# Kernel tuning notes

Hardware: AMD Instinct MI355X
Metric: run time of the kernel (lower is better)

The kernel has to match this reference:

```python
import jax, jax.numpy as jnp
import numpy as np

EPS = 1e-08

def quantize_weights(w):
    # absmean ternary quantization: round(w/delta) clipped to {-1,0,1}, rescaled by delta
    delta = jnp.mean(jnp.abs(w)) + EPS
    w_quant = jnp.clip(jnp.round(w / delta), -1.0, 1.0)
    return w_quant * delta

def setup_inputs() -> dict:
    key = jax.random.key(0)
    k1, k2 = jax.random.split(key)
    B, T, IN, OUT = 8, 16, 4096, 11008
    x = jax.random.normal(k1, (B, T, IN), dtype=jnp.float32)
    weight = jax.random.normal(k2, (OUT, IN), dtype=jnp.float32)
    bias = jnp.zeros((OUT,), dtype=jnp.float32)
    return {"x": x, "weight": weight, "bias": bias}

def reference(x, weight, bias):
    w_quant = quantize_weights(weight)
    # F.linear: x @ w_quant.T + bias
    out = jnp.einsum("bti,oi->bto", x, w_quant) + bias
    return out
```

## Files before the change

### kernel.cpp

```cpp
#include <hip/hip_runtime.h>
#include <hip/hip_bf16.h>

typedef __bf16 bf16x8 __attribute__((ext_vector_type(8)));
typedef float f32x4 __attribute__((ext_vector_type(4)));
typedef unsigned short ushort8 __attribute__((ext_vector_type(8)));
typedef unsigned short ushort4v __attribute__((ext_vector_type(4)));

constexpr int M = 128;
constexpr int K = 4096;
constexpr int N = 11008;
constexpr int BN = 64;
constexpr int BK = 32;
constexpr int KSPLIT = 4;
constexpr int KBLK = K / KSPLIT;
constexpr int NBX = N / BN;
constexpr int NBLK = NBX * KSPLIT;
constexpr long long NW = (long long)N * K;
constexpr size_t MN = (size_t)M * N;
constexpr int SCAP = 512;

constexpr float DHAT = 0.79788456f;
constexpr float INV_DHAT = 1.0f / DHAT;
constexpr float BAND = 2e-4f;
constexpr float DEVMAX = 3.5e-4f;

constexpr size_t PART_OFF  = 0;
constexpr size_t FLAG_OFF  = 4096;
constexpr size_t CNT_OFF   = FLAG_OFF + 4;
constexpr size_t XBF_OFF   = 8192;
constexpr size_t SLIST_OFF = XBF_OFF + (size_t)M * K * 2;
constexpr size_t P_OFF     = SLIST_OFF + (size_t)NBLK * SCAP * 8;
constexpr size_t WS_NEED   = P_OFF + KSPLIT * MN * sizeof(float);
constexpr size_t WS_MIN    = 8192;

__device__ __forceinline__ unsigned short f2bf_bits(float f) {
    unsigned int u = __builtin_bit_cast(unsigned int, f);
    u += 0x7FFFu + ((u >> 16) & 1u);
    return (unsigned short)(u >> 16);
}
__device__ __forceinline__ float bf_to_f32(unsigned short b) {
    return __builtin_bit_cast(float, ((unsigned int)b) << 16);
}
__device__ __forceinline__ int tern(float w, float inv_d) {
    float q = rintf(w * inv_d);
    q = fminf(1.f, fmaxf(-1.f, q));
    return (int)q;
}
__device__ __forceinline__ float block_delta(const float* partials, int tid) {
    __shared__ float red[4];
    float s = 0.f;
    for (int i = tid; i < NBLK; i += 256) s += partials[i];
#pragma unroll
    for (int off = 32; off > 0; off >>= 1) s += __shfl_down(s, off, 64);
    if ((tid & 63) == 0) red[tid >> 6] = s;
    __syncthreads();
    return (float)((double)((red[0] + red[1]) + (red[2] + red[3])) /
                   (double)NW + 1e-8);
}

__global__ __launch_bounds__(256) void xcvt(const float* __restrict__ x,
                                            unsigned short* __restrict__ xbf)
{
    const int gtid = blockIdx.x * blockDim.x + threadIdx.x;
    const float4* xp = (const float4*)x + (size_t)gtid * 2;
    float4 a = xp[0], b = xp[1];
    ushort8 o;
    o[0] = f2bf_bits(a.x); o[1] = f2bf_bits(a.y);
    o[2] = f2bf_bits(a.z); o[3] = f2bf_bits(a.w);
    o[4] = f2bf_bits(b.x); o[5] = f2bf_bits(b.y);
    o[6] = f2bf_bits(b.z); o[7] = f2bf_bits(b.w);
    *(ushort8*)(xbf + (size_t)gtid * 8) = o;
}

__global__ __launch_bounds__(256, 4) void bitlinear_gemm(
    const unsigned short* __restrict__ xb, const float* __restrict__ W,
    float* __restrict__ partials, unsigned int* __restrict__ cnt,
    uint2* __restrict__ slist, unsigned int* __restrict__ flag,
    float* __restrict__ pbase)
{
    constexpr int KSTEPS = KBLK / BK;
    constexpr int LDSW = 40;
    __shared__ __attribute__((aligned(16))) unsigned short xs[2][M * LDSW];
    __shared__ __attribute__((aligned(16))) unsigned short wsm[2][BN * LDSW];
    __shared__ float red[4];

    const int tid = threadIdx.x;
    const int lane = tid & 63;
    const int wid = tid >> 6;
    const int wm = wid >> 1;
    const int wn = wid & 1;
    const int cgrp = lane >> 4;
    const int l15 = lane & 15;
    const int n0 = blockIdx.x * BN;
    const int kk0 = blockIdx.y * KBLK;
    const int bid = blockIdx.y * NBX + blockIdx.x;
    const int K4 = K / 4;
    const float4* w4p = (const float4*)W;
    uint2* mylist = slist + (size_t)bid * SCAP;

    ushort8 xrA[2], xrB[2];
    float4 wrA[2], wrB[2];
    float sabs = 0.f;

    auto issue_set = [&](int t, ushort8 (&xr)[2], float4 (&wr)[2]) {
#pragma unroll
        for (int i = 0; i < 2; ++i) {
            const int j = tid + i * 256;
            xr[i] = *(const ushort8*)(xb + (size_t)(j >> 2) * K + kk0 + t * BK + (j & 3) * 8);
        }
#pragma unroll
        for (int i = 0; i < 2; ++i) {
            const int j = tid + i * 256;
            wr[i] = w4p[(size_t)(n0 + (j >> 3)) * K4 + (kk0 + t * BK) / 4 + (j & 7)];
        }
    };

    auto stage_set = [&](int buf, int t, ushort8 (&xr)[2], float4 (&wr)[2]) {
#pragma unroll
        for (int i = 0; i < 2; ++i) {
            const int j = tid + i * 256;
            *(ushort8*)&xs[buf][(j >> 2) * LDSW + (j & 3) * 8] = xr[i];
        }
#pragma unroll
        for (int i = 0; i < 2; ++i) {
            const int j = tid + i * 256;
            const int row = j >> 3, q4 = j & 7;
            float wf[4] = {wr[i].x, wr[i].y, wr[i].z, wr[i].w};
            ushort4v wq;
            unsigned int msk = 0u;
#pragma unroll
            for (int e = 0; e < 4; ++e) {
                const float r = wf[e] * INV_DHAT;
                float qv = rintf(r);
                qv = fminf(1.f, fmaxf(-1.f, qv));
                wq[e] = f2bf_bits(qv);
                sabs += fabsf(wf[e]);
                msk |= (fabsf(fabsf(r) - 0.5f) < BAND) ? (1u << e) : 0u;
            }
            *(ushort4v*)&wsm[buf][row * LDSW + q4 * 4] = wq;
            if (msk) {
#pragma unroll
                for (int e = 0; e < 4; ++e) {
                    if (msk & (1u << e)) {
                        unsigned int slot = atomicAdd(cnt + bid, 1u);
                        if (slot < SCAP) {
                            unsigned int idx = ((unsigned int)(n0 + row) << 12) |
                                               (unsigned int)(kk0 + t * BK + q4 * 4 + e);
                            mylist[slot] = make_uint2(idx, __float_as_uint(wf[e]));
                        } else {
                            atomicOr(flag, 1u);
                        }
                    }
                }
            }
        }
    };

    f32x4 acc[4][2] = {};

    auto compute = [&](int buf) {
        const unsigned short* xcur = xs[buf];
        const unsigned short* wcur = wsm[buf];
        bf16x8 afr[4], bfr[2];
#pragma unroll
        for (int f = 0; f < 4; ++f)
            afr[f] = *(const bf16x8*)&xcur[(wm * 64 + f * 16 + l15) * LDSW + cgrp * 8];
#pragma unroll
        for (int g = 0; g < 2; ++g)
            bfr[g] = *(const bf16x8*)&wcur[(wn * 32 + g * 16 + l15) * LDSW + cgrp * 8];
#pragma unroll
        for (int f = 0; f < 4; ++f)
#pragma unroll
            for (int g = 0; g < 2; ++g)
                acc[f][g] = __builtin_amdgcn_mfma_f32_16x16x32_bf16(
                    afr[f], bfr[g], acc[f][g], 0, 0, 0);
    };

    issue_set(0, xrA, wrA);
    issue_set(1, xrB, wrB);

    for (int t = 0; t < KSTEPS; t += 2) {
        stage_set(0, t, xrA, wrA);
        if (t + 2 < KSTEPS) issue_set(t + 2, xrA, wrA);
        __syncthreads();
        compute(0);
        stage_set(1, t + 1, xrB, wrB);
        if (t + 3 < KSTEPS) issue_set(t + 3, xrB, wrB);
        __syncthreads();
        compute(1);
    }

#pragma unroll
    for (int off = 32; off > 0; off >>= 1) sabs += __shfl_down(sabs, off, 64);
    if (lane == 0) red[wid] = sabs;
    __syncthreads();
    if (tid == 0) partials[bid] = (red[0] + red[1]) + (red[2] + red[3]);

    float* dst = pbase + (size_t)blockIdx.y * MN;
#pragma unroll
    for (int f = 0; f < 4; ++f) {
        const int mrow = wm * 64 + f * 16 + cgrp * 4;
#pragma unroll
        for (int g = 0; g < 2; ++g) {
            const int ocol = n0 + wn * 32 + g * 16 + l15;
#pragma unroll
            for (int r = 0; r < 4; ++r)
                dst[(size_t)(mrow + r) * N + ocol] = acc[f][g][r];
        }
    }
}

__global__ __launch_bounds__(256) void combine(const float* __restrict__ p,
                                               const float* __restrict__ partials,
                                               const float* __restrict__ bias,
                                               float4* __restrict__ out)
{
    const float delta = block_delta(partials, threadIdx.x);
    const int i4 = blockIdx.x * blockDim.x + threadIdx.x;
    constexpr int N4 = N / 4;
    if (i4 >= (int)(MN / 4)) return;
    const float4 b = *(const float4*)(bias + (i4 % N4) * 4);
    float4 s = {};
#pragma unroll
    for (int y = 0; y < KSPLIT; ++y) {
        float4 v = ((const float4*)(p + y * MN))[i4];
        s.x += v.x; s.y += v.y; s.z += v.z; s.w += v.w;
    }
    float4 o;
    o.x = fmaf(delta, s.x, b.x); o.y = fmaf(delta, s.y, b.y);
    o.z = fmaf(delta, s.z, b.z); o.w = fmaf(delta, s.w, b.w);
    out[i4] = o;
}

__global__ __launch_bounds__(256) void fixup(
    const float* __restrict__ W, const unsigned short* __restrict__ xbf,
    const float* __restrict__ partials, const unsigned int* __restrict__ cnt,
    const uint2* __restrict__ slist, const unsigned int* __restrict__ flag,
    float* __restrict__ out)
{
    const int tid = threadIdx.x;
    const float delta = block_delta(partials, tid);
    const float inv_delta = 1.0f / delta;
    const int bid = blockIdx.y * NBX + blockIdx.x;
    const bool bad = (*flag != 0u) || (fabsf(delta * INV_DHAT - 1.f) > DEVMAX);

    if (!bad) {
        const int cb = (int)min(cnt[bid], (unsigned int)SCAP);
        const uint2* mylist = slist + (size_t)bid * SCAP;
        for (int si = 0; si < cb; ++si) {
            const uint2 e = mylist[si];
            const float w = __uint_as_float(e.y);
            const int dq = tern(w, inv_delta) - tern(w, INV_DHAT);
            if (dq == 0) continue;
            const unsigned int n = e.x >> 12, k = e.x & 4095u;
            const float corr = delta * (float)dq;
            if (tid < M)
                atomicAdd(&out[(size_t)tid * N + n],
                          corr * bf_to_f32(xbf[(size_t)tid * K + k]));
        }
    } else {
        const int n0 = blockIdx.x * BN, kk0 = blockIdx.y * KBLK;
        for (int r = 0; r < BN; ++r) {
            for (int kk = tid; kk < KBLK; kk += 256) {
                const float w = W[(size_t)(n0 + r) * K + kk0 + kk];
                const int dq = tern(w, inv_delta) - tern(w, INV_DHAT);
                if (dq == 0) continue;
                const float corr = delta * (float)dq;
                for (int m = 0; m < M; ++m)
                    atomicAdd(&out[(size_t)m * N + n0 + r],
                              corr * bf_to_f32(xbf[(size_t)m * K + kk0 + kk]));
            }
        }
    }
}

__global__ __launch_bounds__(256) void absmean_direct(const float* __restrict__ w,
                                                      float* __restrict__ partials)
{
    const int gtid = blockIdx.x * blockDim.x + threadIdx.x;
    const int n4 = (int)(NW / 4);
    const float4* w4 = (const float4*)w;
    float s0 = 0.f, s1 = 0.f, s2 = 0.f, s3 = 0.f;
    for (int i = gtid; i < n4; i += gridDim.x * blockDim.x) {
        float4 v = w4[i];
        s0 += fabsf(v.x); s1 += fabsf(v.y); s2 += fabsf(v.z); s3 += fabsf(v.w);
    }
    float s = (s0 + s1) + (s2 + s3);
#pragma unroll
    for (int off = 32; off > 0; off >>= 1) s += __shfl_down(s, off, 64);
    __shared__ float red[4];
    if ((threadIdx.x & 63) == 0) red[threadIdx.x >> 6] = s;
    __syncthreads();
    if (threadIdx.x == 0)
        partials[blockIdx.x] = (red[0] + red[1]) + (red[2] + red[3]);
}

__global__ __launch_bounds__(256, 4) void gemm_direct(
    const float* __restrict__ X, const float* __restrict__ W,
    const float* __restrict__ bias, const float* __restrict__ partials,
    float* __restrict__ out)
{
    constexpr int KSTEPS = K / BK;
    constexpr int LDSW = 40;
    __shared__ __attribute__((aligned(16))) unsigned short xs[2][M * LDSW];
    __shared__ __attribute__((aligned(16))) unsigned short wsm[2][BN * LDSW];
    __shared__ float red[4];
    const int tid = threadIdx.x, lane = tid & 63, wid = tid >> 6;
    const int wm = wid >> 1, wn = wid & 1, cgrp = lane >> 4, l15 = lane & 15;
    const int n0 = blockIdx.x * BN, K4 = K / 4;
    const float4* x4p = (const float4*)X;
    const float4* w4p = (const float4*)W;
    float4 xfA[4], xfB[4], wrA[2], wrB[2];

    auto issue_set = [&](int t, float4 (&xf)[4], float4 (&wr)[2]) {
#pragma unroll
        for (int i = 0; i < 4; ++i) {
            const int j = tid + i * 256;
            xf[i] = x4p[(size_t)(j >> 3) * K4 + (t * BK) / 4 + (j & 7)];
        }
#pragma unroll
        for (int i = 0; i < 2; ++i) {
            const int j = tid + i * 256;
            wr[i] = w4p[(size_t)(n0 + (j >> 3)) * K4 + (t * BK) / 4 + (j & 7)];
        }
    };

    float ps[8];
#pragma unroll
    for (int i = 0; i < 8; ++i) ps[i] = partials[tid + i * 256];
    issue_set(0, xfA, wrA);
    issue_set(1, xfB, wrB);
    float s = 0.f;
#pragma unroll
    for (int i = 0; i < 8; ++i) s += ps[i];
#pragma unroll
    for (int off = 32; off > 0; off >>= 1) s += __shfl_down(s, off, 64);
    if (lane == 0) red[wid] = s;
    __syncthreads();
    const float delta =
        (float)((double)((red[0] + red[1]) + (red[2] + red[3])) / (double)NW + 1e-8);
    const float inv_delta = 1.0f / delta;

    auto stage_set = [&](int buf, float4 (&xf)[4], float4 (&wr)[2]) {
#pragma unroll
        for (int i = 0; i < 4; ++i) {
            const int j = tid + i * 256;
            float4 v = xf[i];
            ushort4v o;
            o[0] = f2bf_bits(v.x); o[1] = f2bf_bits(v.y);
            o[2] = f2bf_bits(v.z); o[3] = f2bf_bits(v.w);
            *(ushort4v*)&xs[buf][(j >> 3) * LDSW + (j & 7) * 4] = o;
        }
#pragma unroll
        for (int i = 0; i < 2; ++i) {
            const int j = tid + i * 256;
            float wf[4] = {wr[i].x, wr[i].y, wr[i].z, wr[i].w};
            ushort4v wq;
#pragma unroll
            for (int e = 0; e < 4; ++e)
                wq[e] = f2bf_bits((float)tern(wf[e], inv_delta));
            *(ushort4v*)&wsm[buf][(j >> 3) * LDSW + (j & 7) * 4] = wq;
        }
    };

    f32x4 acc[4][2] = {};
    auto compute = [&](int buf) {
        bf16x8 afr[4], bfr[2];
#pragma unroll
        for (int f = 0; f < 4; ++f)
            afr[f] = *(const bf16x8*)&xs[buf][(wm * 64 + f * 16 + l15) * LDSW + cgrp * 8];
#pragma unroll
        for (int g = 0; g < 2; ++g)
            bfr[g] = *(const bf16x8*)&wsm[buf][(wn * 32 + g * 16 + l15) * LDSW + cgrp * 8];
#pragma unroll
        for (int f = 0; f < 4; ++f)
#pragma unroll
            for (int g = 0; g < 2; ++g)
                acc[f][g] = __builtin_amdgcn_mfma_f32_16x16x32_bf16(
                    afr[f], bfr[g], acc[f][g], 0, 0, 0);
    };

    for (int t = 0; t < KSTEPS; t += 2) {
        stage_set(0, xfA, wrA);
        if (t + 2 < KSTEPS) issue_set(t + 2, xfA, wrA);
        __syncthreads();
        compute(0);
        stage_set(1, xfB, wrB);
        if (t + 3 < KSTEPS) issue_set(t + 3, xfB, wrB);
        __syncthreads();
        compute(1);
    }
#pragma unroll
    for (int f = 0; f < 4; ++f) {
        const int mrow = wm * 64 + f * 16 + cgrp * 4;
#pragma unroll
        for (int g = 0; g < 2; ++g) {
            const int ocol = n0 + wn * 32 + g * 16 + l15;
            const float bv = bias[ocol];
#pragma unroll
            for (int r = 0; r < 4; ++r)
                out[(size_t)(mrow + r) * N + ocol] = delta * acc[f][g][r] + bv;
        }
    }
}

extern "C" void kernel_launch(void* const* d_in, const int* in_sizes, int n_in,
                              void* d_out, int out_size, void* d_ws, size_t ws_size,
                              hipStream_t stream) {
    const float* x = (const float*)d_in[0];
    const float* w = (const float*)d_in[1];
    const float* bias = (const float*)d_in[2];
    float* out = (float*)d_out;
    char* wsb = (char*)d_ws;
    float* partials = (float*)(wsb + PART_OFF);
    unsigned int* flag = (unsigned int*)(wsb + FLAG_OFF);
    unsigned int* cnt = (unsigned int*)(wsb + CNT_OFF);
    unsigned short* xbf = (unsigned short*)(wsb + XBF_OFF);
    uint2* slist = (uint2*)(wsb + SLIST_OFF);
    float* pbase = (float*)(wsb + P_OFF);

    if (ws_size >= WS_NEED) {
        hipMemsetAsync(wsb + FLAG_OFF, 0, 4 + NBLK * 4, stream);
        xcvt<<<M * K / 8 / 256, 256, 0, stream>>>(x, xbf);
        bitlinear_gemm<<<dim3(NBX, KSPLIT), 256, 0, stream>>>(
            xbf, w, partials, cnt, slist, flag, pbase);
        combine<<<(int)(MN / 4) / 256, 256, 0, stream>>>(
            pbase, partials, bias, (float4*)out);
        fixup<<<dim3(NBX, KSPLIT), 256, 0, stream>>>(
            w, xbf, partials, cnt, slist, flag, out);
    } else if (ws_size >= WS_MIN) {
        absmean_direct<<<2048, 256, 0, stream>>>(w, partials);
        gemm_direct<<<NBX, 256, 0, stream>>>(x, w, bias, partials, out);
    }
}
```

Baseline: 72.82 us.

## Pre-quantize weights to packed 2-bit codes in a streaming prep pass

Result: slower. 87.84 us (+20.6%).

```diff
diff --git a/kernel.cpp b/kernel.cpp
--- a/kernel.cpp
+++ b/kernel.cpp
@@ -14,10 +14,10 @@
 constexpr int KSPLIT = 4;
 constexpr int KBLK = K / KSPLIT;
 constexpr int NBX = N / BN;
-constexpr int NBLK = NBX * KSPLIT;
 constexpr long long NW = (long long)N * K;
+constexpr int RBLK = 2048;
 constexpr size_t MN = (size_t)M * N;
-constexpr int SCAP = 512;
+constexpr int SCAP = 256;
 
 constexpr float DHAT = 0.79788456f;
 constexpr float INV_DHAT = 1.0f / DHAT;
@@ -25,13 +25,14 @@
 constexpr float DEVMAX = 3.5e-4f;
 
 constexpr size_t PART_OFF  = 0;
-constexpr size_t FLAG_OFF  = 4096;
-constexpr size_t CNT_OFF   = FLAG_OFF + 4;
-constexpr size_t XBF_OFF   = 8192;
-constexpr size_t SLIST_OFF = XBF_OFF + (size_t)M * K * 2;
-constexpr size_t P_OFF     = SLIST_OFF + (size_t)NBLK * SCAP * 8;
-constexpr size_t WS_NEED   = P_OFF + KSPLIT * MN * sizeof(float);
-constexpr size_t WS_MIN    = 8192;
+constexpr size_t FLAG_OFF  = 8192;
+constexpr size_t CNT_OFF   = 12288;
+constexpr size_t XBF_OFF   = 24576;
+constexpr size_t CODE_OFF  = XBF_OFF + (size_t)M * K * 2;
+constexpr size_t SLIST_OFF = CODE_OFF + (size_t)(NW / 4);
+constexpr size_t PACC_OFF  = SLIST_OFF + (size_t)RBLK * SCAP * 8;
+constexpr size_t WS_NEED   = PACC_OFF + KSPLIT * MN * sizeof(float);
+constexpr size_t WS_MIN    = 16384;
 
 __device__ __forceinline__ unsigned short f2bf_bits(float f) {
     unsigned int u = __builtin_bit_cast(unsigned int, f);
@@ -49,7 +50,8 @@
 __device__ __forceinline__ float block_delta(const float* partials, int tid) {
     __shared__ float red[4];
     float s = 0.f;
-    for (int i = tid; i < NBLK; i += 256) s += partials[i];
+#pragma unroll
+    for (int i = 0; i < RBLK / 256; ++i) s += partials[tid + i * 256];
 #pragma unroll
     for (int off = 32; off > 0; off >>= 1) s += __shfl_down(s, off, 64);
     if ((tid & 63) == 0) red[tid >> 6] = s;
@@ -58,31 +60,82 @@
                    (double)NW + 1e-8);
 }
 
-__global__ __launch_bounds__(256) void xcvt(const float* __restrict__ x,
-                                            unsigned short* __restrict__ xbf)
+template <bool CVT>
+__global__ __launch_bounds__(256) void prep(const float* __restrict__ w,
+                                            const float* __restrict__ x,
+                                            float* __restrict__ partials,
+                                            unsigned short* __restrict__ xbf,
+                                            unsigned char* __restrict__ codes,
+                                            unsigned int* __restrict__ cnt,
+                                            uint2* __restrict__ slist,
+                                            unsigned int* __restrict__ flag)
 {
     const int gtid = blockIdx.x * blockDim.x + threadIdx.x;
-    const float4* xp = (const float4*)x + (size_t)gtid * 2;
-    float4 a = xp[0], b = xp[1];
-    ushort8 o;
-    o[0] = f2bf_bits(a.x); o[1] = f2bf_bits(a.y);
-    o[2] = f2bf_bits(a.z); o[3] = f2bf_bits(a.w);
-    o[4] = f2bf_bits(b.x); o[5] = f2bf_bits(b.y);
-    o[6] = f2bf_bits(b.z); o[7] = f2bf_bits(b.w);
-    *(ushort8*)(xbf + (size_t)gtid * 8) = o;
-}
-
-__global__ __launch_bounds__(256, 4) void bitlinear_gemm(
-    const unsigned short* __restrict__ xb, const float* __restrict__ W,
-    float* __restrict__ partials, unsigned int* __restrict__ cnt,
-    uint2* __restrict__ slist, unsigned int* __restrict__ flag,
+    if (CVT && gtid < M * K / 8) {
+        const float4* xp = (const float4*)x + (size_t)gtid * 2;
+        float4 a = xp[0], b = xp[1];
+        ushort8 o;
+        o[0] = f2bf_bits(a.x); o[1] = f2bf_bits(a.y);
+        o[2] = f2bf_bits(a.z); o[3] = f2bf_bits(a.w);
+        o[4] = f2bf_bits(b.x); o[5] = f2bf_bits(b.y);
+        o[6] = f2bf_bits(b.z); o[7] = f2bf_bits(b.w);
+        *(ushort8*)(xbf + (size_t)gtid * 8) = o;
+    }
+    const int n4 = (int)(NW / 4);
+    const float4* w4 = (const float4*)w;
+    uint2* mylist = slist + (size_t)blockIdx.x * SCAP;
+    const int stride = gridDim.x * blockDim.x;
+
+    float s0 = 0.f, s1 = 0.f, s2 = 0.f, s3 = 0.f;
+    for (int i = gtid; i < n4; i += stride) {
+        float4 v = w4[i];
+        s0 += fabsf(v.x); s1 += fabsf(v.y); s2 += fabsf(v.z); s3 += fabsf(v.w);
+        if (CVT) {
+            float vf[4] = {v.x, v.y, v.z, v.w};
+            unsigned int byte = 0u, msk = 0u;
+#pragma unroll
+            for (int e = 0; e < 4; ++e) {
+                const float r = vf[e] * INV_DHAT;
+                float qv = rintf(r);
+                qv = fminf(1.f, fmaxf(-1.f, qv));
+                const int iq = (int)qv;
+                byte |= ((unsigned int)iq & 3u) << (2 * e);
+                msk |= (fabsf(fabsf(r) - 0.5f) < BAND) ? (1u << e) : 0u;
+            }
+            codes[i] = (unsigned char)byte;
+            if (msk) {
+#pragma unroll
+                for (int e = 0; e < 4; ++e) {
+                    if (msk & (1u << e)) {
+                        unsigned int slot = atomicAdd(cnt + blockIdx.x, 1u);
+                        if (slot < SCAP)
+                            mylist[slot] = make_uint2(4u * (unsigned)i + e,
+                                                      __float_as_uint(vf[e]));
+                        else
+                            atomicOr(flag, 1u);
+                    }
+                }
+            }
+        }
+    }
+    float s = (s0 + s1) + (s2 + s3);
+#pragma unroll
+    for (int off = 32; off > 0; off >>= 1) s += __shfl_down(s, off, 64);
+    __shared__ float red[4];
+    if ((threadIdx.x & 63) == 0) red[threadIdx.x >> 6] = s;
+    __syncthreads();
+    if (threadIdx.x == 0)
+        partials[blockIdx.x] = (red[0] + red[1]) + (red[2] + red[3]);
+}
+
+__global__ __launch_bounds__(256, 4) void gemm_codes(
+    const unsigned short* __restrict__ xb, const unsigned short* __restrict__ c16,
     float* __restrict__ pbase)
 {
     constexpr int KSTEPS = KBLK / BK;
     constexpr int LDSW = 40;
     __shared__ __attribute__((aligned(16))) unsigned short xs[2][M * LDSW];
     __shared__ __attribute__((aligned(16))) unsigned short wsm[2][BN * LDSW];
-    __shared__ float red[4];
 
     const int tid = threadIdx.x;
     const int lane = tid & 63;
@@ -93,81 +146,45 @@
     const int l15 = lane & 15;
     const int n0 = blockIdx.x * BN;
     const int kk0 = blockIdx.y * KBLK;
-    const int bid = blockIdx.y * NBX + blockIdx.x;
-    const int K4 = K / 4;
-    const float4* w4p = (const float4*)W;
-    uint2* mylist = slist + (size_t)bid * SCAP;
+    const int K8 = K / 8;
 
     ushort8 xrA[2], xrB[2];
-    float4 wrA[2], wrB[2];
-    float sabs = 0.f;
-
-    auto issue_set = [&](int t, ushort8 (&xr)[2], float4 (&wr)[2]) {
+    unsigned int crA, crB;
+
+    auto issue_set = [&](int t, ushort8 (&xr)[2], unsigned int& cr) {
 #pragma unroll
         for (int i = 0; i < 2; ++i) {
             const int j = tid + i * 256;
             xr[i] = *(const ushort8*)(xb + (size_t)(j >> 2) * K + kk0 + t * BK + (j & 3) * 8);
         }
+        cr = c16[(size_t)(n0 + (tid >> 2)) * K8 + (kk0 + t * BK) / 8 + (tid & 3)];
+    };
+
+    auto stage_set = [&](int buf, ushort8 (&xr)[2], unsigned int cr) {
 #pragma unroll
         for (int i = 0; i < 2; ++i) {
             const int j = tid + i * 256;
-            wr[i] = w4p[(size_t)(n0 + (j >> 3)) * K4 + (kk0 + t * BK) / 4 + (j & 7)];
-        }
-    };
-
-    auto stage_set = [&](int buf, int t, ushort8 (&xr)[2], float4 (&wr)[2]) {
-#pragma unroll
-        for (int i = 0; i < 2; ++i) {
-            const int j = tid + i * 256;
             *(ushort8*)&xs[buf][(j >> 2) * LDSW + (j & 3) * 8] = xr[i];
         }
-#pragma unroll
-        for (int i = 0; i < 2; ++i) {
-            const int j = tid + i * 256;
-            const int row = j >> 3, q4 = j & 7;
-            float wf[4] = {wr[i].x, wr[i].y, wr[i].z, wr[i].w};
-            ushort4v wq;
-            unsigned int msk = 0u;
-#pragma unroll
-            for (int e = 0; e < 4; ++e) {
-                const float r = wf[e] * INV_DHAT;
-                float qv = rintf(r);
-                qv = fminf(1.f, fmaxf(-1.f, qv));
-                wq[e] = f2bf_bits(qv);
-                sabs += fabsf(wf[e]);
-                msk |= (fabsf(fabsf(r) - 0.5f) < BAND) ? (1u << e) : 0u;
-            }
-            *(ushort4v*)&wsm[buf][row * LDSW + q4 * 4] = wq;
-            if (msk) {
-#pragma unroll
-                for (int e = 0; e < 4; ++e) {
-                    if (msk & (1u << e)) {
-                        unsigned int slot = atomicAdd(cnt + bid, 1u);
-                        if (slot < SCAP) {
-                            unsigned int idx = ((unsigned int)(n0 + row) << 12) |
-                                               (unsigned int)(kk0 + t * BK + q4 * 4 + e);
-                            mylist[slot] = make_uint2(idx, __float_as_uint(wf[e]));
-                        } else {
-                            atomicOr(flag, 1u);
-                        }
-                    }
-                }
-            }
-        }
+        ushort8 wq;
+#pragma unroll
+        for (int e = 0; e < 8; ++e) {
+            const unsigned int c = (cr >> (2 * e)) & 3u;
+            wq[e] = (unsigned short)(((c & 1u) * 0x3F80u) | ((c & 2u) << 14));
+        }
+        *(ushort8*)&wsm[buf][(tid >> 2) * LDSW + (tid & 3) * 8] = wq;
     };
 
     f32x4 acc[4][2] = {};
 
     auto compute = [&](int buf) {
-        const unsigned short* xcur = xs[buf];
-        const unsigned short* wcur = wsm[buf];
         bf16x8 afr[4], bfr[2];
 #pragma unroll
         for (int f = 0; f < 4; ++f)
-            afr[f] = *(const bf16x8*)&xcur[(wm * 64 + f * 16 + l15) * LDSW + cgrp * 8];
+            afr[f] = *(const bf16x8*)&xs[buf][(wm * 64 + f * 16 + l15) * LDSW + cgrp * 8];
 #pragma unroll
         for (int g = 0; g < 2; ++g)
-            bfr[g] = *(const bf16x8*)&wcur[(wn * 32 + g * 16 + l15) * LDSW + cgrp * 8];
+            bfr[g] = *(const bf16x8*)&wsm[buf][(wn * 32 + g * 16 + l15) * LDSW + cgrp * 8];
 #pragma unroll
         for (int f = 0; f < 4; ++f)
 #pragma unroll
@@ -176,25 +193,19 @@
                     afr[f], bfr[g], acc[f][g], 0, 0, 0);
     };
 
-    issue_set(0, xrA, wrA);
-    issue_set(1, xrB, wrB);
+    issue_set(0, xrA, crA);
+    issue_set(1, xrB, crB);
 
     for (int t = 0; t < KSTEPS; t += 2) {
-        stage_set(0, t, xrA, wrA);
-        if (t + 2 < KSTEPS) issue_set(t + 2, xrA, wrA);
+        stage_set(0, xrA, crA);
+        if (t + 2 < KSTEPS) issue_set(t + 2, xrA, crA);
         __syncthreads();
         compute(0);
-        stage_set(1, t + 1, xrB, wrB);
-        if (t + 3 < KSTEPS) issue_set(t + 3, xrB, wrB);
+        stage_set(1, xrB, crB);
+        if (t + 3 < KSTEPS) issue_set(t + 3, xrB, crB);
         __syncthreads();
         compute(1);
     }
-
-#pragma unroll
-    for (int off = 32; off > 0; off >>= 1) sabs += __shfl_down(sabs, off, 64);
-    if (lane == 0) red[wid] = sabs;
-    __syncthreads();
-    if (tid == 0) partials[bid] = (red[0] + red[1]) + (red[2] + red[3]);
 
     float* dst = pbase + (size_t)blockIdx.y * MN;
 #pragma unroll
@@ -241,12 +252,11 @@
     const int tid = threadIdx.x;
     const float delta = block_delta(partials, tid);
     const float inv_delta = 1.0f / delta;
-    const int bid = blockIdx.y * NBX + blockIdx.x;
     const bool bad = (*flag != 0u) || (fabsf(delta * INV_DHAT - 1.f) > DEVMAX);
 
     if (!bad) {
-        const int cb = (int)min(cnt[bid], (unsigned int)SCAP);
-        const uint2* mylist = slist + (size_t)bid * SCAP;
+        const int cb = (int)min(cnt[blockIdx.x], (unsigned int)SCAP);
+        const uint2* mylist = slist + (size_t)blockIdx.x * SCAP;
         for (int si = 0; si < cb; ++si) {
             const uint2 e = mylist[si];
             const float w = __uint_as_float(e.y);
@@ -259,16 +269,22 @@
                           corr * bf_to_f32(xbf[(size_t)tid * K + k]));
         }
     } else {
-        const int n0 = blockIdx.x * BN, kk0 = blockIdx.y * KBLK;
-        for (int r = 0; r < BN; ++r) {
-            for (int kk = tid; kk < KBLK; kk += 256) {
-                const float w = W[(size_t)(n0 + r) * K + kk0 + kk];
-                const int dq = tern(w, inv_delta) - tern(w, INV_DHAT);
+        const int n4 = (int)(NW / 4);
+        const float4* w4 = (const float4*)W;
+        const int stride = gridDim.x * blockDim.x;
+        for (int i = blockIdx.x * blockDim.x + tid; i < n4; i += stride) {
+            float4 v = w4[i];
+            float vf[4] = {v.x, v.y, v.z, v.w};
+#pragma unroll
+            for (int e = 0; e < 4; ++e) {
+                const int dq = tern(vf[e], inv_delta) - tern(vf[e], INV_DHAT);
                 if (dq == 0) continue;
+                const unsigned int flat = 4u * (unsigned)i + e;
+                const unsigned int n = flat >> 12, k = flat & 4095u;
                 const float corr = delta * (float)dq;
                 for (int m = 0; m < M; ++m)
-                    atomicAdd(&out[(size_t)m * N + n0 + r],
-                              corr * bf_to_f32(xbf[(size_t)m * K + kk0 + kk]));
+                    atomicAdd(&out[(size_t)m * N + n],
+                              corr * bf_to_f32(xbf[(size_t)m * K + k]));
             }
         }
     }
@@ -302,7 +318,7 @@
 {
     constexpr int KSTEPS = K / BK;
     constexpr int LDSW = 40;
-    __shared__ __attribute__((aligned(16))) unsigned short xs[2][M * LDSW];
+    __shared__ __attribute__((aligned(16))) unsigned short xsl[2][M * LDSW];
     __shared__ __attribute__((aligned(16))) unsigned short wsm[2][BN * LDSW];
     __shared__ float red[4];
     const int tid = threadIdx.x, lane = tid & 63, wid = tid >> 6;
@@ -349,7 +365,7 @@
             ushort4v o;
             o[0] = f2bf_bits(v.x); o[1] = f2bf_bits(v.y);
             o[2] = f2bf_bits(v.z); o[3] = f2bf_bits(v.w);
-            *(ushort4v*)&xs[buf][(j >> 3) * LDSW + (j & 7) * 4] = o;
+            *(ushort4v*)&xsl[buf][(j >> 3) * LDSW + (j & 7) * 4] = o;
         }
 #pragma unroll
         for (int i = 0; i < 2; ++i) {
@@ -368,7 +384,7 @@
         bf16x8 afr[4], bfr[2];
 #pragma unroll
         for (int f = 0; f < 4; ++f)
-            afr[f] = *(const bf16x8*)&xs[buf][(wm * 64 + f * 16 + l15) * LDSW + cgrp * 8];
+            afr[f] = *(const bf16x8*)&xsl[buf][(wm * 64 + f * 16 + l15) * LDSW + cgrp * 8];
 #pragma unroll
         for (int g = 0; g < 2; ++g)
             bfr[g] = *(const bf16x8*)&wsm[buf][(wn * 32 + g * 16 + l15) * LDSW + cgrp * 8];
@@ -416,19 +432,21 @@
     unsigned int* flag = (unsigned int*)(wsb + FLAG_OFF);
     unsigned int* cnt = (unsigned int*)(wsb + CNT_OFF);
     unsigned short* xbf = (unsigned short*)(wsb + XBF_OFF);
+    unsigned char* codes = (unsigned char*)(wsb + CODE_OFF);
     uint2* slist = (uint2*)(wsb + SLIST_OFF);
-    float* pbase = (float*)(wsb + P_OFF);
+    float* pacc = (float*)(wsb + PACC_OFF);
 
     if (ws_size >= WS_NEED) {
-        hipMemsetAsync(wsb + FLAG_OFF, 0, 4 + NBLK * 4, stream);
-        xcvt<<<M * K / 8 / 256, 256, 0, stream>>>(x, xbf);
-        bitlinear_gemm<<<dim3(NBX, KSPLIT), 256, 0, stream>>>(
-            xbf, w, partials, cnt, slist, flag, pbase);
-        combine<<<(int)(MN / 4) / 256, 256, 0, stream>>>(
-            pbase, partials, bias, (float4*)out);
-        fixup<<<dim3(NBX, KSPLIT), 256, 0, stream>>>(
-            w, xbf, partials, cnt, slist, flag, out);
-    } else if (ws_size >= WS_MIN) {
+        hipMemsetAsync(wsb + FLAG_OFF, 0, 4, stream);
+        hipMemsetAsync(wsb + CNT_OFF, 0, (size_t)RBLK * 4, stream);
+        prep<true><<<RBLK, 256, 0, stream>>>(w, x, partials, xbf, codes,
+                                             cnt, slist, flag);
+        gemm_codes<<<dim3(NBX, KSPLIT), 256, 0, stream>>>(
+            xbf, (const unsigned short*)codes, pacc);
+        combine<<<(int)(MN / 4 + 255) / 256, 256, 0, stream>>>(
+            pacc, partials, bias, (float4*)out);
+        fixup<<<RBLK, 256, 0, stream>>>(w, xbf, partials, cnt, slist, flag, out);
+    } else {
         absmean_direct<<<2048, 256, 0, stream>>>(w, partials);
         gemm_direct<<<NBX, 256, 0, stream>>>(x, w, bias, partials, out);
     }
```
